# Performance work log

Hardware: AMD Instinct MI355X
Metric: run time of the kernel (lower is better)

Reference implementation:

```python
import jax, jax.numpy as jnp
import numpy as np

H = 8
SPLIT = 1
# deterministic stand-in for random.shuffle(range(8)) in the original
_PERM = np.random.RandomState(0).permutation(H)
SERIES_IDX = jnp.asarray(_PERM[SPLIT:])  # 7 heads
CROSS_IDX = jnp.asarray(_PERM[:SPLIT])   # 1 head


def setup_inputs() -> dict:
    key = jax.random.key(0)
    ks = jax.random.split(key, 5)
    B, L, E = 8, 1024, 64
    shp = (B, L, H, E)
    return {
        "queries": jax.random.normal(ks[0], shp, dtype=jnp.float32),
        "keys": jax.random.normal(ks[1], shp, dtype=jnp.float32),
        "keysT": jax.random.normal(ks[2], shp, dtype=jnp.float32),
        "values": jax.random.normal(ks[3], shp, dtype=jnp.float32),
        "valuesT": jax.random.normal(ks[4], shp, dtype=jnp.float32),
    }


def reference(queries, keys, keysT, values, valuesT):
    B, L, _, E = queries.shape
    scale = 1.0 / jnp.sqrt(jnp.asarray(E, dtype=queries.dtype))
    neg_inf = jnp.asarray(-jnp.inf, dtype=queries.dtype)

    # head split (gather along head dim)
    sq = queries[:, :, SERIES_IDX]   # [B,L,7,E]
    sk = keys[:, :, SERIES_IDX]      # [B,S,7,E]
    sv = values[:, :, SERIES_IDX]    # [B,S,7,D]
    cq = queries[:, :, CROSS_IDX]    # [B,L,1,E]
    ckT = keysT[:, :, CROSS_IDX]     # [B,C,1,E]
    cvT = valuesT[:, :, CROSS_IDX]   # [B,C,1,D]

    # causal mask: True above the diagonal -> disallowed
    causal = jnp.triu(jnp.ones((L, L), dtype=bool), k=1)  # [L,L]

    # series branch
    scores = jnp.einsum('blne,bsne->bnls', sq, sk)  # [B,7,L,S]
    scores = jnp.where(causal[None, None], neg_inf, scores * scale)
    series = jax.nn.softmax(scores, axis=-1)
    V = jnp.einsum('bhls,bshd->blhd', series, sv)   # [B,L,7,D]

    # cross branch
    cscores = jnp.einsum('blme,bcme->bmlc', cq, ckT)  # [B,1,L,C]
    cscores = jnp.where(causal[None, None], neg_inf, cscores * scale)
    crosses = jax.nn.softmax(cscores, axis=-1)
    V_cross = jnp.einsum('bhlc,bchd->blhd', crosses, cvT)  # [B,L,1,D]

    return jnp.concatenate([V, V_cross], axis=2)  # [B,L,8,D]
```

## Files before the change

### kernel.cpp

```cpp
#include <hip/hip_runtime.h>
#include <math.h>

#define Lq 1024
#define Hq 8
#define Eq 64
#define LDW 72
#define KV_SH (64 * LDW)
#define BUF_SH (2 * KV_SH)

#define SRC_HEAD_PACKED 0x64503712u

typedef __bf16 bf16_t;
typedef __bf16 bf16x8 __attribute__((ext_vector_type(8)));
typedef __bf16 bf16x4 __attribute__((ext_vector_type(4)));
typedef short short4v __attribute__((ext_vector_type(4)));
typedef float floatx4 __attribute__((ext_vector_type(4)));

__device__ __forceinline__ bf16x8 cvt8(const float4 a, const float4 b) {
    bf16x8 r;
    r[0] = (bf16_t)a.x; r[1] = (bf16_t)a.y; r[2] = (bf16_t)a.z; r[3] = (bf16_t)a.w;
    r[4] = (bf16_t)b.x; r[5] = (bf16_t)b.y; r[6] = (bf16_t)b.z; r[7] = (bf16_t)b.w;
    return r;
}

__device__ __forceinline__ void block_sync_lds() {
    asm volatile("s_waitcnt lgkmcnt(0)" ::: "memory");
    __builtin_amdgcn_s_barrier();
    __builtin_amdgcn_sched_barrier(0);
}

__global__ __launch_bounds__(256, 2)
void attn_mfma(const float* __restrict__ Q, const float* __restrict__ Ks,
               const float* __restrict__ KTs, const float* __restrict__ Vs,
               const float* __restrict__ VTs, float* __restrict__ out) {
    const int slot = blockIdx.x;
    const int b    = blockIdx.y;
    const int qt   = 15 - blockIdx.z;
    const int h    = (SRC_HEAD_PACKED >> (slot * 4)) & 0xF;
    const float* __restrict__ Kp = (slot == 7) ? KTs : Ks;
    const float* __restrict__ Vp = (slot == 7) ? VTs : Vs;

    const int tid  = threadIdx.x;
    const int wv   = tid >> 6;
    const int lane = tid & 63;
    const int ln16 = lane & 15;
    const int quad = lane >> 4;
    const int kh   = wv & 1;
    const int wh   = wv >> 1;

    __shared__ alignas(16) unsigned short smem[2 * BUF_SH];

    const float qs = 0.125f * 1.44269504f;
    bf16x8 qf[2][2];
    #pragma unroll
    for (int qi = 0; qi < 2; ++qi) {
        const int qg = wh * 2 + qi;
        const int r = qt * 64 + qg * 16 + ln16;
        const float* qa = Q + (((size_t)b * Lq + r) * Hq + h) * Eq + quad * 8;
        #pragma unroll
        for (int ec = 0; ec < 2; ++ec) {
            float4 f0 = ((const float4*)(qa + ec * 32))[0];
            float4 f1 = ((const float4*)(qa + ec * 32))[1];
            f0.x*=qs; f0.y*=qs; f0.z*=qs; f0.w*=qs;
            f1.x*=qs; f1.y*=qs; f1.z*=qs; f1.w*=qs;
            qf[qi][ec] = cvt8(f0, f1);
        }
    }

    floatx4 O[2][4];
    #pragma unroll
    for (int qi = 0; qi < 2; ++qi)
        #pragma unroll
        for (int dc = 0; dc < 4; ++dc) O[qi][dc] = (floatx4){0, 0, 0, 0};
    float psl[2] = {0.f, 0.f};

    float4 kq[4];
    float  vq[16];
    const int kj = tid >> 2, kc = (tid & 3) * 16;
    const int vd = lane,     vk = wv * 16;

    auto load_tile = [&](int kt) {
        const float* kb = Kp + (((size_t)b * Lq + kt * 64 + kj) * Hq + h) * Eq + kc;
        kq[0] = ((const float4*)kb)[0]; kq[1] = ((const float4*)kb)[1];
        kq[2] = ((const float4*)kb)[2]; kq[3] = ((const float4*)kb)[3];
        const float* vb = Vp + (((size_t)b * Lq + kt * 64 + vk) * Hq + h) * Eq + vd;
        #pragma unroll
        for (int i = 0; i < 16; ++i) vq[i] = vb[(size_t)i * (Hq * Eq)];
    };
    auto stage = [&](int bsel) {
        unsigned short* dst = smem + bsel * BUF_SH;
        *(bf16x8*)&dst[kj * LDW + kc]     = cvt8(kq[0], kq[1]);
        *(bf16x8*)&dst[kj * LDW + kc + 8] = cvt8(kq[2], kq[3]);
        const float4* vq4 = (const float4*)vq;
        *(bf16x8*)&dst[KV_SH + vd * LDW + vk]     = cvt8(vq4[0], vq4[1]);
        *(bf16x8*)&dst[KV_SH + vd * LDW + vk + 8] = cvt8(vq4[2], vq4[3]);
    };

    load_tile(0);
    stage(0);
    load_tile(1);
    block_sync_lds();

    for (int kt = 0; kt <= qt; ++kt) {
        const unsigned short* base = smem + (kt & 1) * BUF_SH;

        bf16x8 kf[2][2];
        #pragma unroll
        for (int c = 0; c < 2; ++c) {
            kf[c][0] = *(const bf16x8*)&base[((kh * 2 + c) * 16 + ln16) * LDW + quad * 8];
            kf[c][1] = *(const bf16x8*)&base[((kh * 2 + c) * 16 + ln16) * LDW + 32 + quad * 8];
        }
        if (kt < qt) stage((kt + 1) & 1);
        if (kt + 1 < qt) load_tile(kt + 2);

        bf16x4 va[4][2];
        #pragma unroll
        for (int dc = 0; dc < 4; ++dc)
            #pragma unroll
            for (int nc = 0; nc < 2; ++nc)
                va[dc][nc] = *(const bf16x4*)&base[KV_SH + (dc * 16 + ln16) * LDW + kh * 32 + nc * 16 + quad * 4];

        const bool diag = (kt == qt);
        #pragma unroll
        for (int qi = 0; qi < 2; ++qi) {
            const int qg = wh * 2 + qi;
            if (diag && kh && wh == 0) continue;

            floatx4 s[2];
            #pragma unroll
            for (int nc = 0; nc < 2; ++nc) {
                floatx4 acc = (floatx4){0, 0, 0, 0};
                acc = __builtin_amdgcn_mfma_f32_16x16x32_bf16(kf[nc][0], qf[qi][0], acc, 0, 0, 0);
                acc = __builtin_amdgcn_mfma_f32_16x16x32_bf16(kf[nc][1], qf[qi][1], acc, 0, 0, 0);
                s[nc] = acc;
            }
            if (diag) {
                const int rin = qg * 16 + ln16;
                #pragma unroll
                for (int nc = 0; nc < 2; ++nc)
                    #pragma unroll
                    for (int r = 0; r < 4; ++r)
                        if (kh * 32 + nc * 16 + quad * 4 + r > rin) s[nc][r] = -INFINITY;
            }
            float pv[2][4];
            float ps = 0.f;
            #pragma unroll
            for (int nc = 0; nc < 2; ++nc)
                #pragma unroll
                for (int r = 0; r < 4; ++r) {
                    pv[nc][r] = __builtin_amdgcn_exp2f(s[nc][r]);
                    ps += pv[nc][r];
                }
            psl[qi] += ps;

            short4v pb[2];
            #pragma unroll
            for (int nc = 0; nc < 2; ++nc) {
                bf16x4 t;
                t[0] = (bf16_t)pv[nc][0]; t[1] = (bf16_t)pv[nc][1];
                t[2] = (bf16_t)pv[nc][2]; t[3] = (bf16_t)pv[nc][3];
                pb[nc] = __builtin_bit_cast(short4v, t);
            }
            #pragma unroll
            for (int dc = 0; dc < 4; ++dc)
                #pragma unroll
                for (int nc = 0; nc < 2; ++nc)
                    O[qi][dc] = __builtin_amdgcn_mfma_f32_16x16x16bf16_1k(
                        __builtin_bit_cast(short4v, va[dc][nc]), pb[nc], O[qi][dc], 0, 0, 0);
        }
        block_sync_lds();
    }

    float lsum[2];
    #pragma unroll
    for (int qi = 0; qi < 2; ++qi) {
        float l = psl[qi];
        l += __shfl_xor(l, 16, 64);
        l += __shfl_xor(l, 32, 64);
        lsum[qi] = l;
    }

    float* mb = (float*)smem;
    if (kh) {
        #pragma unroll
        for (int qi = 0; qi < 2; ++qi) {
            const int qg = wh * 2 + qi;
            float* dst = mb + (qg * 64 + lane) * 18;
            #pragma unroll
            for (int dc = 0; dc < 4; ++dc) {
                *(float2*)(dst + dc * 4)     = make_float2(O[qi][dc][0], O[qi][dc][1]);
                *(float2*)(dst + dc * 4 + 2) = make_float2(O[qi][dc][2], O[qi][dc][3]);
            }
            dst[16] = lsum[qi];
        }
    }
    __syncthreads();
    if (!kh) {
        #pragma unroll
        for (int qi = 0; qi < 2; ++qi) {
            const int qg = wh * 2 + qi;
            const float* src = mb + (qg * 64 + lane) * 18;
            const float inv = 1.0f / (lsum[qi] + src[16]);
            const int row = qt * 64 + qg * 16 + ln16;
            float* op = out + (((size_t)b * Lq + row) * Hq + slot) * Eq + quad * 4;
            #pragma unroll
            for (int dc = 0; dc < 4; ++dc) {
                float4 o;
                o.x = (O[qi][dc][0] + src[dc * 4 + 0]) * inv;
                o.y = (O[qi][dc][1] + src[dc * 4 + 1]) * inv;
                o.z = (O[qi][dc][2] + src[dc * 4 + 2]) * inv;
                o.w = (O[qi][dc][3] + src[dc * 4 + 3]) * inv;
                *(float4*)(op + dc * 16) = o;
            }
        }
    }
}

extern "C" void kernel_launch(void* const* d_in, const int* in_sizes, int n_in,
                              void* d_out, int out_size, void* d_ws, size_t ws_size,
                              hipStream_t stream) {
    const float* queries = (const float*)d_in[0];
    const float* keys    = (const float*)d_in[1];
    const float* keysT   = (const float*)d_in[2];
    const float* values  = (const float*)d_in[3];
    const float* valuesT = (const float*)d_in[4];
    float* out = (float*)d_out;

    dim3 grid(Hq, 8, 16);
    dim3 block(256);
    attn_mfma<<<grid, block, 0, stream>>>(queries, keys, keysT, values, valuesT, out);
}
```

Baseline: 130.9 us.

## Pair complementary causal query tiles per block to share K/V staging

Each 512-thread block now handles two query tiles, p and 15-p, with the two 256-thread halves each computing one tile. Both halves share a single K/V tile stream staged into shared memory. This balances causal work across blocks and halves the global K/V loads for the shorter tile. The trade-off is idle waves in the half that finishes early while the longer tile continues, barriers across more threads, and a grid with half as many blocks.

```diff
diff --git a/kernel.cpp b/kernel.cpp
--- a/kernel.cpp
+++ b/kernel.cpp
@@ -29,24 +29,27 @@
     __builtin_amdgcn_sched_barrier(0);
 }
 
-__global__ __launch_bounds__(256, 2)
+__global__ __launch_bounds__(512, 4)
 void attn_mfma(const float* __restrict__ Q, const float* __restrict__ Ks,
                const float* __restrict__ KTs, const float* __restrict__ Vs,
                const float* __restrict__ VTs, float* __restrict__ out) {
     const int slot = blockIdx.x;
     const int b    = blockIdx.y;
-    const int qt   = 15 - blockIdx.z;
+    const int p    = blockIdx.z;
     const int h    = (SRC_HEAD_PACKED >> (slot * 4)) & 0xF;
     const float* __restrict__ Kp = (slot == 7) ? KTs : Ks;
     const float* __restrict__ Vp = (slot == 7) ? VTs : Vs;
+    const int pA = p, pB = 15 - p;
 
     const int tid  = threadIdx.x;
     const int wv   = tid >> 6;
     const int lane = tid & 63;
     const int ln16 = lane & 15;
     const int quad = lane >> 4;
-    const int kh   = wv & 1;
-    const int wh   = wv >> 1;
+    const int tb   = wv >> 2;
+    const int kh   = (wv >> 1) & 1;
+    const int wh   = wv & 1;
+    const int pT   = tb ? pB : pA;
 
     __shared__ alignas(16) unsigned short smem[2 * BUF_SH];
 
@@ -55,7 +58,7 @@
     #pragma unroll
     for (int qi = 0; qi < 2; ++qi) {
         const int qg = wh * 2 + qi;
-        const int r = qt * 64 + qg * 16 + ln16;
+        const int r = pT * 64 + qg * 16 + ln16;
         const float* qa = Q + (((size_t)b * Lq + r) * Hq + h) * Eq + quad * 8;
         #pragma unroll
         for (int ec = 0; ec < 2; ++ec) {
@@ -74,26 +77,23 @@
         for (int dc = 0; dc < 4; ++dc) O[qi][dc] = (floatx4){0, 0, 0, 0};
     float psl[2] = {0.f, 0.f};
 
-    float4 kq[4];
-    float  vq[16];
-    const int kj = tid >> 2, kc = (tid & 3) * 16;
-    const int vd = lane,     vk = wv * 16;
+    float4 kq[2];
+    float  vq[8];
+    const int kj = tid >> 3, kc = (tid & 7) * 8;
+    const int vd = tid & 63, vk = (tid >> 6) * 8;
 
     auto load_tile = [&](int kt) {
         const float* kb = Kp + (((size_t)b * Lq + kt * 64 + kj) * Hq + h) * Eq + kc;
         kq[0] = ((const float4*)kb)[0]; kq[1] = ((const float4*)kb)[1];
-        kq[2] = ((const float4*)kb)[2]; kq[3] = ((const float4*)kb)[3];
         const float* vb = Vp + (((size_t)b * Lq + kt * 64 + vk) * Hq + h) * Eq + vd;
         #pragma unroll
-        for (int i = 0; i < 16; ++i) vq[i] = vb[(size_t)i * (Hq * Eq)];
+        for (int i = 0; i < 8; ++i) vq[i] = vb[(size_t)i * (Hq * Eq)];
     };
     auto stage = [&](int bsel) {
         unsigned short* dst = smem + bsel * BUF_SH;
-        *(bf16x8*)&dst[kj * LDW + kc]     = cvt8(kq[0], kq[1]);
-        *(bf16x8*)&dst[kj * LDW + kc + 8] = cvt8(kq[2], kq[3]);
+        *(bf16x8*)&dst[kj * LDW + kc] = cvt8(kq[0], kq[1]);
         const float4* vq4 = (const float4*)vq;
-        *(bf16x8*)&dst[KV_SH + vd * LDW + vk]     = cvt8(vq4[0], vq4[1]);
-        *(bf16x8*)&dst[KV_SH + vd * LDW + vk + 8] = cvt8(vq4[2], vq4[3]);
+        *(bf16x8*)&dst[KV_SH + vd * LDW + vk] = cvt8(vq4[0], vq4[1]);
     };
 
     load_tile(0);
@@ -101,72 +101,77 @@
     load_tile(1);
     block_sync_lds();
 
-    for (int kt = 0; kt <= qt; ++kt) {
+    for (int kt = 0; kt <= pB; ++kt) {
         const unsigned short* base = smem + (kt & 1) * BUF_SH;
+        const bool act = (kt <= pT);
 
         bf16x8 kf[2][2];
-        #pragma unroll
-        for (int c = 0; c < 2; ++c) {
-            kf[c][0] = *(const bf16x8*)&base[((kh * 2 + c) * 16 + ln16) * LDW + quad * 8];
-            kf[c][1] = *(const bf16x8*)&base[((kh * 2 + c) * 16 + ln16) * LDW + 32 + quad * 8];
-        }
-        if (kt < qt) stage((kt + 1) & 1);
-        if (kt + 1 < qt) load_tile(kt + 2);
-
-        bf16x4 va[4][2];
-        #pragma unroll
-        for (int dc = 0; dc < 4; ++dc)
-            #pragma unroll
-            for (int nc = 0; nc < 2; ++nc)
-                va[dc][nc] = *(const bf16x4*)&base[KV_SH + (dc * 16 + ln16) * LDW + kh * 32 + nc * 16 + quad * 4];
-
-        const bool diag = (kt == qt);
-        #pragma unroll
-        for (int qi = 0; qi < 2; ++qi) {
-            const int qg = wh * 2 + qi;
-            if (diag && kh && wh == 0) continue;
-
-            floatx4 s[2];
-            #pragma unroll
-            for (int nc = 0; nc < 2; ++nc) {
-                floatx4 acc = (floatx4){0, 0, 0, 0};
-                acc = __builtin_amdgcn_mfma_f32_16x16x32_bf16(kf[nc][0], qf[qi][0], acc, 0, 0, 0);
-                acc = __builtin_amdgcn_mfma_f32_16x16x32_bf16(kf[nc][1], qf[qi][1], acc, 0, 0, 0);
-                s[nc] = acc;
-            }
-            if (diag) {
-                const int rin = qg * 16 + ln16;
+        if (act) {
+            #pragma unroll
+            for (int c = 0; c < 2; ++c) {
+                kf[c][0] = *(const bf16x8*)&base[((kh * 2 + c) * 16 + ln16) * LDW + quad * 8];
+                kf[c][1] = *(const bf16x8*)&base[((kh * 2 + c) * 16 + ln16) * LDW + 32 + quad * 8];
+            }
+        }
+        if (kt < pB) stage((kt + 1) & 1);
+        if (kt + 1 < pB) load_tile(kt + 2);
+
+        if (act) {
+            bf16x4 va[4][2];
+            #pragma unroll
+            for (int dc = 0; dc < 4; ++dc)
+                #pragma unroll
+                for (int nc = 0; nc < 2; ++nc)
+                    va[dc][nc] = *(const bf16x4*)&base[KV_SH + (dc * 16 + ln16) * LDW + kh * 32 + nc * 16 + quad * 4];
+
+            const bool diag = (kt == pT);
+            #pragma unroll
+            for (int qi = 0; qi < 2; ++qi) {
+                const int qg = wh * 2 + qi;
+                if (diag && kh && wh == 0) continue;
+
+                floatx4 s[2];
+                #pragma unroll
+                for (int nc = 0; nc < 2; ++nc) {
+                    floatx4 acc = (floatx4){0, 0, 0, 0};
+                    acc = __builtin_amdgcn_mfma_f32_16x16x32_bf16(kf[nc][0], qf[qi][0], acc, 0, 0, 0);
+                    acc = __builtin_amdgcn_mfma_f32_16x16x32_bf16(kf[nc][1], qf[qi][1], acc, 0, 0, 0);
+                    s[nc] = acc;
+                }
+                if (diag) {
+                    const int rin = qg * 16 + ln16;
+                    #pragma unroll
+                    for (int nc = 0; nc < 2; ++nc)
+                        #pragma unroll
+                        for (int r = 0; r < 4; ++r)
+                            if (kh * 32 + nc * 16 + quad * 4 + r > rin) s[nc][r] = -INFINITY;
+                }
+                float pv[2][4];
+                float ps = 0.f;
                 #pragma unroll
                 for (int nc = 0; nc < 2; ++nc)
                     #pragma unroll
-                    for (int r = 0; r < 4; ++r)
-                        if (kh * 32 + nc * 16 + quad * 4 + r > rin) s[nc][r] = -INFINITY;
-            }
-            float pv[2][4];
-            float ps = 0.f;
-            #pragma unroll
-            for (int nc = 0; nc < 2; ++nc)
-                #pragma unroll
-                for (int r = 0; r < 4; ++r) {
-                    pv[nc][r] = __builtin_amdgcn_exp2f(s[nc][r]);
-                    ps += pv[nc][r];
+                    for (int r = 0; r < 4; ++r) {
+                        pv[nc][r] = __builtin_amdgcn_exp2f(s[nc][r]);
+                        ps += pv[nc][r];
+                    }
+                psl[qi] += ps;
+
+                short4v pb[2];
+                #pragma unroll
+                for (int nc = 0; nc < 2; ++nc) {
+                    bf16x4 t;
+                    t[0] = (bf16_t)pv[nc][0]; t[1] = (bf16_t)pv[nc][1];
+                    t[2] = (bf16_t)pv[nc][2]; t[3] = (bf16_t)pv[nc][3];
+                    pb[nc] = __builtin_bit_cast(short4v, t);
                 }
-            psl[qi] += ps;
-
-            short4v pb[2];
-            #pragma unroll
-            for (int nc = 0; nc < 2; ++nc) {
-                bf16x4 t;
-                t[0] = (bf16_t)pv[nc][0]; t[1] = (bf16_t)pv[nc][1];
-                t[2] = (bf16_t)pv[nc][2]; t[3] = (bf16_t)pv[nc][3];
-                pb[nc] = __builtin_bit_cast(short4v, t);
-            }
-            #pragma unroll
-            for (int dc = 0; dc < 4; ++dc)
-                #pragma unroll
-                for (int nc = 0; nc < 2; ++nc)
-                    O[qi][dc] = __builtin_amdgcn_mfma_f32_16x16x16bf16_1k(
-                        __builtin_bit_cast(short4v, va[dc][nc]), pb[nc], O[qi][dc], 0, 0, 0);
+                #pragma unroll
+                for (int dc = 0; dc < 4; ++dc)
+                    #pragma unroll
+                    for (int nc = 0; nc < 2; ++nc)
+                        O[qi][dc] = __builtin_amdgcn_mfma_f32_16x16x16bf16_1k(
+                            __builtin_bit_cast(short4v, va[dc][nc]), pb[nc], O[qi][dc], 0, 0, 0);
+            }
         }
         block_sync_lds();
     }
@@ -185,7 +190,7 @@
         #pragma unroll
         for (int qi = 0; qi < 2; ++qi) {
             const int qg = wh * 2 + qi;
-            float* dst = mb + (qg * 64 + lane) * 18;
+            float* dst = mb + ((tb * 4 + qg) * 64 + lane) * 18;
             #pragma unroll
             for (int dc = 0; dc < 4; ++dc) {
                 *(float2*)(dst + dc * 4)     = make_float2(O[qi][dc][0], O[qi][dc][1]);
@@ -199,9 +204,9 @@
         #pragma unroll
         for (int qi = 0; qi < 2; ++qi) {
             const int qg = wh * 2 + qi;
-            const float* src = mb + (qg * 64 + lane) * 18;
+            const float* src = mb + ((tb * 4 + qg) * 64 + lane) * 18;
             const float inv = 1.0f / (lsum[qi] + src[16]);
-            const int row = qt * 64 + qg * 16 + ln16;
+            const int row = pT * 64 + qg * 16 + ln16;
             float* op = out + (((size_t)b * Lq + row) * Hq + slot) * Eq + quad * 4;
             #pragma unroll
             for (int dc = 0; dc < 4; ++dc) {
@@ -226,7 +231,7 @@
     const float* valuesT = (const float*)d_in[4];
     float* out = (float*)d_out;
 
-    dim3 grid(Hq, 8, 16);
-    dim3 block(256);
+    dim3 grid(Hq, 8, 8);
+    dim3 block(512);
     attn_mfma<<<grid, block, 0, stream>>>(queries, keys, keysT, values, valuesT, out);
 }
```

Result: faster. 127.2 us, median of 2 (-2.9%).
